# Optimization experiments

Hardware: AMD Instinct MI355X
Metric: run time of the kernel (lower is better)

Reference implementation:

```python
import jax, jax.numpy as jnp
import numpy as np

N_NODES = 100000
N_EDGES = 1600000
NFEAT, NHID, NCLASS = 128, 64, 40


def setup_inputs() -> dict:
    key = jax.random.key(0)
    k = jax.random.split(key, 6)
    x = jax.random.normal(k[0], (N_NODES, NFEAT), dtype=jnp.float32)
    edge_index = jax.random.randint(k[1], (2, N_EDGES), 0, N_NODES, dtype=jnp.int64)
    edge_weight = jax.random.uniform(k[2], (N_EDGES,), dtype=jnp.float32)
    # Glorot-style init as in PyG GCNConv.reset_parameters
    W1 = jax.random.normal(k[3], (NFEAT, NHID), dtype=jnp.float32) * (1.0 / np.sqrt(NFEAT))
    b1 = jnp.zeros((NHID,), dtype=jnp.float32)
    W2 = jax.random.normal(k[4], (NHID, NCLASS), dtype=jnp.float32) * (1.0 / np.sqrt(NHID))
    b2 = jnp.zeros((NCLASS,), dtype=jnp.float32)
    return {"x": x, "edge_index": edge_index, "edge_weight": edge_weight,
            "W1": W1, "b1": b1, "W2": W2, "b2": b2}


def _gcn_conv(x, edge_index, edge_weight, W, b):
    """PyG GCNConv: add self-loops, symmetric gcn_norm, linear, scatter-add, bias."""
    n = x.shape[0]
    loop = jnp.arange(n)
    row = jnp.concatenate([edge_index[0], loop])  # source nodes
    col = jnp.concatenate([edge_index[1], loop])  # target nodes
    w = jnp.concatenate([edge_weight, jnp.ones((n,), edge_weight.dtype)])
    deg = jax.ops.segment_sum(w, col, num_segments=n)          # [N]
    dinv = jnp.where(deg > 0, jax.lax.rsqrt(deg), 0.0)
    norm = dinv[row] * w * dinv[col]                           # [E+N]
    h = x @ W                                                  # [N, out]
    msg = norm[:, None] * h[row]                               # gather: [E+N, out]
    out = jax.ops.segment_sum(msg, col, num_segments=n)        # scatter-add: [N, out]
    return out + b


def reference(x, edge_index, edge_weight, W1, b1, W2, b2):
    h = jax.nn.relu(_gcn_conv(x, edge_index, edge_weight, W1, b1))
    # F.dropout with training=False is identity (eval mode)
    return _gcn_conv(h, edge_index, edge_weight, W2, b2)
```

## Files before the change

kernel.cpp:

```cpp
#include <hip/hip_runtime.h>
#include <hip/hip_bf16.h>

#define N_NODES 100000
#define N_EDGES 1600000
#define NFEAT 128
#define NHID 64
#define NCLASS 40
#define CAP 64

#define BIN_SHIFT 9
#define BIN_NODES 512
#define NBIN ((N_NODES + BIN_NODES - 1) / BIN_NODES)
#define SCAP 10240
#define CHUNK 4096
#define EPT 16
#define BIN_BLOCKS ((N_EDGES + CHUNK - 1) / CHUNK)
#define GEMM1_BLOCKS ((N_NODES + 63) / 64)

using frag_ab = __attribute__((ext_vector_type(8))) short;
using frag_cd = __attribute__((ext_vector_type(4))) float;


__device__ __forceinline__ unsigned pack2(float a, float b) {
    unsigned ua = __float_as_uint(a), ub = __float_as_uint(b);
    unsigned ra = (ua + 0x7FFFu + ((ua >> 16) & 1u)) >> 16;
    unsigned rb = (ub + 0x7FFFu + ((ub >> 16) & 1u)) >> 16;
    return ra | (rb << 16);
}
__device__ __forceinline__ unsigned short bf16rtn(float f) {
    unsigned u = __float_as_uint(f);
    return (unsigned short)((u + 0x7FFFu + ((u >> 16) & 1u)) >> 16);
}
__device__ __forceinline__ float lo16(unsigned w) { return __uint_as_float(w << 16); }
__device__ __forceinline__ float hi16(unsigned w) { return __uint_as_float(w & 0xFFFF0000u); }


__global__ __launch_bounds__(256) void fusedA_kernel(
        const int* __restrict__ ei, const float* __restrict__ ew,
        int* __restrict__ bincnt, uint2* __restrict__ staging,
        const float* __restrict__ x, const float* __restrict__ W1,
        unsigned short* __restrict__ h1b) {
    __shared__ unsigned short sm[16384];
    int t = threadIdx.x;

    if (blockIdx.x < BIN_BLOCKS) {
        int* lcnt  = (int*)sm;
        int* gbase = lcnt + NBIN;
        for (int i = t; i < NBIN; i += 256) lcnt[i] = 0;
        __syncthreads();

        int base = blockIdx.x * CHUNK;
        int c[EPT]; unsigned en[EPT];
#pragma unroll
        for (int u = 0; u < EPT; ++u) {
            int e = base + u * 256 + t;
            if (e < N_EDGES) {
                c[u] = ei[N_EDGES + e];
                unsigned wq = (unsigned)fminf(ew[e] * 32768.0f, 32767.0f);
                en[u] = ((unsigned)ei[e] << 15) | wq;
            } else {
                c[u] = -1;
            }
        }
#pragma unroll
        for (int u = 0; u < EPT; ++u)
            if (c[u] >= 0) atomicAdd(&lcnt[c[u] >> BIN_SHIFT], 1);
        __syncthreads();
        if (t < NBIN) {
            int n = lcnt[t];
            gbase[t] = (n > 0) ? atomicAdd(&bincnt[t], n) : 0;
        }
        __syncthreads();
        if (t < NBIN) lcnt[t] = 0;
        __syncthreads();
#pragma unroll
        for (int u = 0; u < EPT; ++u) {
            if (c[u] >= 0) {
                int b = c[u] >> BIN_SHIFT;
                int p = gbase[b] + atomicAdd(&lcnt[b], 1);
                if (p < SCAP)
                    staging[(size_t)b * SCAP + p] = make_uint2(en[u], (unsigned)c[u]);
            }
        }
        return;
    }

    int row0 = (blockIdx.x - BIN_BLOCKS) * 64;

#pragma unroll
    for (int p = 0; p < 4; ++p) {
        int id = p * 256 + t;
        int r = id >> 4;
        int c = id & 15;
        int gr = row0 + r; if (gr > N_NODES - 1) gr = N_NODES - 1;
        const float* src = x + (size_t)gr * NFEAT + c * 8;
        float4 f0 = *(const float4*)src;
        float4 f1 = *(const float4*)(src + 4);
        uint4 pk = make_uint4(pack2(f0.x, f0.y), pack2(f0.z, f0.w),
                              pack2(f1.x, f1.y), pack2(f1.z, f1.w));
        int cs = c ^ (r & 15);
        *(uint4*)(&sm[r * 128 + cs * 8]) = pk;
    }
#pragma unroll
    for (int p = 0; p < 4; ++p) {
        int id = p * 256 + t;
        int n = id >> 4;
        int c = id & 15;
        const float* wsrc = W1 + (size_t)(c * 8) * NHID + n;
        uint4 pk = make_uint4(pack2(wsrc[0 * NHID], wsrc[1 * NHID]),
                              pack2(wsrc[2 * NHID], wsrc[3 * NHID]),
                              pack2(wsrc[4 * NHID], wsrc[5 * NHID]),
                              pack2(wsrc[6 * NHID], wsrc[7 * NHID]));
        int cs = c ^ (n & 15);
        *(uint4*)(&sm[8192 + n * 128 + cs * 8]) = pk;
    }
    __syncthreads();

    int w = t >> 6, l = t & 63;
    int li = l & 15, q = l >> 4;
    int arow = w * 16 + li;

    frag_cd acc0 = {0.f, 0.f, 0.f, 0.f};
    frag_cd acc1 = {0.f, 0.f, 0.f, 0.f};
    frag_cd acc2 = {0.f, 0.f, 0.f, 0.f};
    frag_cd acc3 = {0.f, 0.f, 0.f, 0.f};

#pragma unroll
    for (int kc = 0; kc < 4; ++kc) {
        int cc = (kc * 4 + q) ^ li;
        frag_ab a  = *(const frag_ab*)(&sm[arow * 128 + cc * 8]);
        frag_ab b0 = *(const frag_ab*)(&sm[8192 + (0 * 16 + li) * 128 + cc * 8]);
        frag_ab b1 = *(const frag_ab*)(&sm[8192 + (1 * 16 + li) * 128 + cc * 8]);
        frag_ab b2 = *(const frag_ab*)(&sm[8192 + (2 * 16 + li) * 128 + cc * 8]);
        frag_ab b3 = *(const frag_ab*)(&sm[8192 + (3 * 16 + li) * 128 + cc * 8]);
        acc0 = __builtin_amdgcn_mfma_f32_16x16x32_bf16(a, b0, acc0, 0, 0, 0);
        acc1 = __builtin_amdgcn_mfma_f32_16x16x32_bf16(a, b1, acc1, 0, 0, 0);
        acc2 = __builtin_amdgcn_mfma_f32_16x16x32_bf16(a, b2, acc2, 0, 0, 0);
        acc3 = __builtin_amdgcn_mfma_f32_16x16x32_bf16(a, b3, acc3, 0, 0, 0);
    }

#pragma unroll
    for (int reg = 0; reg < 4; ++reg) {
        int rrow = row0 + w * 16 + q * 4 + reg;
        if (rrow < N_NODES) {
            unsigned short* dst = h1b + (size_t)rrow * NHID + li;
            dst[0]  = bf16rtn(acc0[reg]);
            dst[16] = bf16rtn(acc1[reg]);
            dst[32] = bf16rtn(acc2[reg]);
            dst[48] = bf16rtn(acc3[reg]);
        }
    }
}


__global__ __launch_bounds__(512) void place_kernel(const int* __restrict__ bincnt,
                                                    const uint2* __restrict__ staging,
                                                    unsigned* __restrict__ bucket,
                                                    int* __restrict__ cnt,
                                                    float* __restrict__ dinv,
                                                    int* __restrict__ ghist) {
    __shared__ int lpos[BIN_NODES];
    __shared__ float lws[BIN_NODES];
    __shared__ int lhist[CAP + 1];
    int b = blockIdx.x;
    int t = threadIdx.x;
    for (int i = t; i < BIN_NODES; i += 512) { lpos[i] = 0; lws[i] = 0.0f; }
    if (t <= CAP) lhist[t] = 0;
    __syncthreads();

    int nodebase = b << BIN_SHIFT;
    int n = bincnt[b];
    if (n > SCAP) n = SCAP;
    const uint2* st = staging + (size_t)b * SCAP;
    for (int i = t; i < n; i += 512) {
        uint2 en = st[i];
        int local = (int)en.y - nodebase;
        int p = atomicAdd(&lpos[local], 1);
        if (p < CAP) bucket[((size_t)en.y << 6) + p] = en.x;
        atomicAdd(&lws[local], (float)(en.x & 32767u) * (1.0f / 32768.0f));
    }
    __syncthreads();
    for (int i = t; i < BIN_NODES; i += 512) {
        int node = nodebase + i;
        if (node < N_NODES) {
            int d = min(lpos[i], CAP);
            cnt[node] = d;
            dinv[node] = rsqrtf(1.0f + lws[i]);
            atomicAdd(&lhist[d], 1);
        }
    }
    __syncthreads();
    if (t <= CAP) { int h = lhist[t]; if (h) atomicAdd(&ghist[t], h); }
}


__global__ __launch_bounds__(512) void perm_kernel(const int* __restrict__ cnt,
                                                   const int* __restrict__ ghist,
                                                   int* __restrict__ goffs,
                                                   int* __restrict__ perm) {
    __shared__ int base[CAP + 1];
    __shared__ int lh[CAP + 1];
    __shared__ int lbase[CAP + 1];
    int t = threadIdx.x;
    if (t <= CAP) lh[t] = 0;
    if (t == 0) {
        int s = 0;
        for (int d = 0; d <= CAP; ++d) { base[d] = s; s += ghist[d]; }
    }
    __syncthreads();
    int node = blockIdx.x * 512 + t;
    bool v = node < N_NODES;
    int d = 0, rank = 0;
    if (v) { d = cnt[node]; rank = atomicAdd(&lh[d], 1); }
    __syncthreads();
    if (t <= CAP) { int h = lh[t]; lbase[t] = h ? atomicAdd(&goffs[t], h) : 0; }
    __syncthreads();
    if (v) perm[base[d] + lbase[d] + rank] = node;
}


__global__ __launch_bounds__(256) void gather1_kernel(
        const int* __restrict__ cnt, const unsigned* __restrict__ bucket,
        const float* __restrict__ dinv, const unsigned short* __restrict__ h1b,
        const float* __restrict__ b1, unsigned short* __restrict__ relu1b,
        const int* __restrict__ perm) {
    int t = threadIdx.x;
    int lane = t & 63;
    int wave = t >> 6;
    int g = lane >> 3;
    int l = lane & 7;
    int slot = (blockIdx.x * 4 + wave) * 8 + g;
    bool nvalid = slot < N_NODES;
    int node = perm[nvalid ? slot : 0];
    int d = cnt[node];
    float dc = dinv[node];

    uint4 eb0 = *(const uint4*)(bucket + ((size_t)node << 6) + l * 8);
    uint4 eb1 = *(const uint4*)(bucket + ((size_t)node << 6) + l * 8 + 4);
    int rl[8]; float wl[8];
#pragma unroll
    for (int k = 0; k < 8; ++k) {
        unsigned e = (k < 4) ? ((const unsigned*)&eb0)[k] : ((const unsigned*)&eb1)[k - 4];
        int sl = l * 8 + k;
        bool ok = sl < d;
        int r = ok ? (int)(e >> 15) : 0;
        rl[k] = r;
        wl[k] = ok ? (float)(e & 32767u) * (1.0f / 32768.0f) * dinv[r] : 0.0f;
    }

    uint4 hs = *(const uint4*)(h1b + (size_t)node * NHID + l * 8);
    float acc[8];
#pragma unroll
    for (int k = 0; k < 4; ++k) {
        unsigned w = ((const unsigned*)&hs)[k];
        acc[2 * k] = dc * lo16(w);
        acc[2 * k + 1] = dc * hi16(w);
    }

    for (int j = 0; j < d; j += 8) {
        int src = (g << 3) + (j >> 3);
        int r[8]; float w[8];
#pragma unroll
        for (int k = 0; k < 8; ++k) { r[k] = __shfl(rl[k], src); w[k] = __shfl(wl[k], src); }
        uint4 v[8];
#pragma unroll
        for (int k = 0; k < 8; ++k)
            v[k] = *(const uint4*)(h1b + (size_t)r[k] * NHID + l * 8);
#pragma unroll
        for (int k = 0; k < 8; ++k) {
#pragma unroll
            for (int q = 0; q < 4; ++q) {
                unsigned ww = ((const unsigned*)&v[k])[q];
                acc[2 * q] += w[k] * lo16(ww);
                acc[2 * q + 1] += w[k] * hi16(ww);
            }
        }
    }
    if (nvalid) {
        float4 bv0 = *(const float4*)(b1 + l * 8);
        float4 bv1 = *(const float4*)(b1 + l * 8 + 4);
        float o0 = fmaxf(dc * acc[0] + bv0.x, 0.0f), o1 = fmaxf(dc * acc[1] + bv0.y, 0.0f);
        float o2 = fmaxf(dc * acc[2] + bv0.z, 0.0f), o3 = fmaxf(dc * acc[3] + bv0.w, 0.0f);
        float o4 = fmaxf(dc * acc[4] + bv1.x, 0.0f), o5 = fmaxf(dc * acc[5] + bv1.y, 0.0f);
        float o6 = fmaxf(dc * acc[6] + bv1.z, 0.0f), o7 = fmaxf(dc * acc[7] + bv1.w, 0.0f);
        uint4 pk = make_uint4(pack2(o0, o1), pack2(o2, o3), pack2(o4, o5), pack2(o6, o7));
        *(uint4*)(relu1b + (size_t)node * NHID + l * 8) = pk;
    }
}


__global__ __launch_bounds__(256) void gemm2_kernel(const unsigned short* __restrict__ relu1b,
                                                    const float* __restrict__ W2,
                                                    unsigned short* __restrict__ h2b) {
    __shared__ unsigned short sa[64 * 64];
    __shared__ unsigned short sb[48 * 64];
    int t = threadIdx.x;
    int row0 = blockIdx.x * 64;

#pragma unroll
    for (int p = 0; p < 2; ++p) {
        int id = p * 256 + t;
        int r = id >> 3, cj = id & 7;
        int gr = row0 + r; if (gr > N_NODES - 1) gr = N_NODES - 1;
        uint4 v = *(const uint4*)(relu1b + (size_t)gr * NHID + cj * 8);
        int cs = cj ^ (r & 7);
        *(uint4*)(&sa[r * 64 + cs * 8]) = v;
    }
    for (int id = t; id < 384; id += 256) {
        int n = id >> 3, cj = id & 7;
        uint4 v = make_uint4(0u, 0u, 0u, 0u);
        if (n < NCLASS) {
            const float* wsrc = W2 + (size_t)(cj * 8) * NCLASS + n;
            v = make_uint4(pack2(wsrc[0 * NCLASS], wsrc[1 * NCLASS]),
                           pack2(wsrc[2 * NCLASS], wsrc[3 * NCLASS]),
                           pack2(wsrc[4 * NCLASS], wsrc[5 * NCLASS]),
                           pack2(wsrc[6 * NCLASS], wsrc[7 * NCLASS]));
        }
        int cs = cj ^ (n & 7);
        *(uint4*)(&sb[n * 64 + cs * 8]) = v;
    }
    __syncthreads();

    int w = t >> 6, l = t & 63;
    int li = l & 15, q = l >> 4;
    int arow = w * 16 + li;

    frag_cd acc0 = {0.f, 0.f, 0.f, 0.f};
    frag_cd acc1 = {0.f, 0.f, 0.f, 0.f};
    frag_cd acc2 = {0.f, 0.f, 0.f, 0.f};

#pragma unroll
    for (int kc = 0; kc < 2; ++kc) {
        int cc = (kc * 4 + q) ^ (li & 7);
        frag_ab a  = *(const frag_ab*)(&sa[arow * 64 + cc * 8]);
        frag_ab b0 = *(const frag_ab*)(&sb[(0 + li) * 64 + cc * 8]);
        frag_ab b1 = *(const frag_ab*)(&sb[(16 + li) * 64 + cc * 8]);
        frag_ab b2 = *(const frag_ab*)(&sb[(32 + li) * 64 + cc * 8]);
        acc0 = __builtin_amdgcn_mfma_f32_16x16x32_bf16(a, b0, acc0, 0, 0, 0);
        acc1 = __builtin_amdgcn_mfma_f32_16x16x32_bf16(a, b1, acc1, 0, 0, 0);
        acc2 = __builtin_amdgcn_mfma_f32_16x16x32_bf16(a, b2, acc2, 0, 0, 0);
    }

#pragma unroll
    for (int reg = 0; reg < 4; ++reg) {
        int rrow = row0 + w * 16 + q * 4 + reg;
        if (rrow < N_NODES) {
            unsigned short* dst = h2b + (size_t)rrow * NCLASS;
            dst[li] = bf16rtn(acc0[reg]);
            dst[16 + li] = bf16rtn(acc1[reg]);
            if (li < 8) dst[32 + li] = bf16rtn(acc2[reg]);
        }
    }
}


__global__ __launch_bounds__(256) void gather2_kernel(
        const int* __restrict__ cnt, const unsigned* __restrict__ bucket,
        const float* __restrict__ dinv, const unsigned short* __restrict__ h2b,
        const float* __restrict__ b2, float* __restrict__ out,
        const int* __restrict__ perm) {
    int t = threadIdx.x;
    int lane = t & 63;
    int wave = t >> 6;
    int g = lane >> 4;
    int l = lane & 15;
    int slot = (blockIdx.x * 4 + wave) * 4 + g;
    bool nvalid = slot < N_NODES;
    int node = perm[nvalid ? slot : 0];
    int d = cnt[node];
    float dc = dinv[node];
    bool fvalid = (l < 10);

    uint4 eb = *(const uint4*)(bucket + ((size_t)node << 6) + l * 4);
    int rl[4]; float wl[4];
#pragma unroll
    for (int k = 0; k < 4; ++k) {
        unsigned e = ((const unsigned*)&eb)[k];
        int sl = l * 4 + k;
        bool ok = sl < d;
        int r = ok ? (int)(e >> 15) : 0;
        rl[k] = r;
        wl[k] = ok ? (float)(e & 32767u) * (1.0f / 32768.0f) * dinv[r] : 0.0f;
    }

    float acc[4] = {};
    int lc = fvalid ? l * 4 : 0;
    if (fvalid) {
        uint2 hs = *(const uint2*)(h2b + (size_t)node * NCLASS + lc);
        acc[0] = dc * lo16(hs.x); acc[1] = dc * hi16(hs.x);
        acc[2] = dc * lo16(hs.y); acc[3] = dc * hi16(hs.y);
    }

    for (int j = 0; j < d; j += 4) {
        int src = (g << 4) + (j >> 2);
        int r0 = __shfl(rl[0], src), r1 = __shfl(rl[1], src);
        int r2 = __shfl(rl[2], src), r3 = __shfl(rl[3], src);
        float w0 = __shfl(wl[0], src), w1 = __shfl(wl[1], src);
        float w2 = __shfl(wl[2], src), w3 = __shfl(wl[3], src);
        if (fvalid) {
            uint2 v0 = *(const uint2*)(h2b + (size_t)r0 * NCLASS + lc);
            uint2 v1 = *(const uint2*)(h2b + (size_t)r1 * NCLASS + lc);
            uint2 v2 = *(const uint2*)(h2b + (size_t)r2 * NCLASS + lc);
            uint2 v3 = *(const uint2*)(h2b + (size_t)r3 * NCLASS + lc);
            acc[0] += w0 * lo16(v0.x) + w1 * lo16(v1.x) + w2 * lo16(v2.x) + w3 * lo16(v3.x);
            acc[1] += w0 * hi16(v0.x) + w1 * hi16(v1.x) + w2 * hi16(v2.x) + w3 * hi16(v3.x);
            acc[2] += w0 * lo16(v0.y) + w1 * lo16(v1.y) + w2 * lo16(v2.y) + w3 * lo16(v3.y);
            acc[3] += w0 * hi16(v0.y) + w1 * hi16(v1.y) + w2 * hi16(v2.y) + w3 * hi16(v3.y);
        }
    }
    if (nvalid && fvalid) {
        float4 bv = *(const float4*)(b2 + l * 4);
        *(float4*)(out + (size_t)node * NCLASS + l * 4) =
            make_float4(dc * acc[0] + bv.x, dc * acc[1] + bv.y,
                        dc * acc[2] + bv.z, dc * acc[3] + bv.w);
    }
}


extern "C" void kernel_launch(void* const* d_in, const int* in_sizes, int n_in,
                              void* d_out, int out_size, void* d_ws, size_t ws_size,
                              hipStream_t stream) {
    const float* x  = (const float*)d_in[0];
    const int*   ei = (const int*)d_in[1];
    const float* ew = (const float*)d_in[2];
    const float* W1 = (const float*)d_in[3];
    const float* b1 = (const float*)d_in[4];
    const float* W2 = (const float*)d_in[5];
    const float* b2 = (const float*)d_in[6];
    float* out = (float*)d_out;

    int*            bincnt  = (int*)d_ws;
    int*            ghist   = bincnt + 256;
    int*            goffs   = ghist + 65;
    int*            cnt     = bincnt + 512;
    float*          dinv    = (float*)(cnt + 100352);
    unsigned*       bucket  = (unsigned*)(dinv + 100352);
    unsigned short* h1b     = (unsigned short*)(bucket + (size_t)N_NODES * CAP);
    unsigned short* region2 = h1b + (size_t)N_NODES * NHID;
    uint2*          staging = (uint2*)region2;
    unsigned short* relu1b  = region2;
    int*            perm    = (int*)(relu1b + (size_t)N_NODES * NHID);
    unsigned short* h2b     = h1b;

    hipMemsetAsync(bincnt, 0, 512 * sizeof(int), stream);

    fusedA_kernel<<<BIN_BLOCKS + GEMM1_BLOCKS, 256, 0, stream>>>(
        ei, ew, bincnt, staging, x, W1, h1b);
    place_kernel<<<NBIN, 512, 0, stream>>>(bincnt, staging, bucket, cnt, dinv, ghist);
    perm_kernel<<<NBIN, 512, 0, stream>>>(cnt, ghist, goffs, perm);

    gather1_kernel<<<(N_NODES + 31) / 32, 256, 0, stream>>>(
        cnt, bucket, dinv, h1b, b1, relu1b, perm);

    gemm2_kernel<<<(N_NODES + 63) / 64, 256, 0, stream>>>(relu1b, W2, h2b);
    gather2_kernel<<<(N_NODES + 15) / 16, 256, 0, stream>>>(
        cnt, bucket, dinv, h2b, b2, out, perm);
}
```

Measured before the change: 255.7 us.

## Fuse layer-1 gather with layer-2 GEMM and split binning from GEMM1

The layer-1 aggregation now writes its ReLU output as a bf16 tile into shared memory, and the same block immediately runs the W2 MFMA product. The result is scattered to h2b through perm, so the relu1b round trip through global memory and a kernel launch both go away. The fused binning+GEMM1 kernel is split back into separate bin and gemm1 kernels. This removes the branch divergence between block types but loses any overlap the fused launch gave, and each g1g2 block reloads W2 into shared memory.

```diff
diff --git a/kernel.cpp b/kernel.cpp
--- a/kernel.cpp
+++ b/kernel.cpp
@@ -14,8 +14,6 @@
 #define SCAP 10240
 #define CHUNK 4096
 #define EPT 16
-#define BIN_BLOCKS ((N_EDGES + CHUNK - 1) / CHUNK)
-#define GEMM1_BLOCKS ((N_NODES + 63) / 64)
 
 using frag_ab = __attribute__((ext_vector_type(8))) short;
 using frag_cd = __attribute__((ext_vector_type(4))) float;
@@ -35,57 +33,124 @@
 __device__ __forceinline__ float hi16(unsigned w) { return __uint_as_float(w & 0xFFFF0000u); }
 
 
-__global__ __launch_bounds__(256) void fusedA_kernel(
-        const int* __restrict__ ei, const float* __restrict__ ew,
-        int* __restrict__ bincnt, uint2* __restrict__ staging,
-        const float* __restrict__ x, const float* __restrict__ W1,
-        unsigned short* __restrict__ h1b) {
+__global__ __launch_bounds__(256) void bin_kernel(const int* __restrict__ ei,
+                                                  const float* __restrict__ ew,
+                                                  int* __restrict__ bincnt,
+                                                  uint2* __restrict__ staging) {
+    __shared__ int lcnt[NBIN];
+    __shared__ int gbase[NBIN];
+    int t = threadIdx.x;
+    for (int i = t; i < NBIN; i += 256) lcnt[i] = 0;
+    __syncthreads();
+
+    int base = blockIdx.x * CHUNK;
+    int c[EPT]; unsigned en[EPT];
+#pragma unroll
+    for (int u = 0; u < EPT; ++u) {
+        int e = base + u * 256 + t;
+        if (e < N_EDGES) {
+            c[u] = ei[N_EDGES + e];
+            unsigned wq = (unsigned)fminf(ew[e] * 32768.0f, 32767.0f);
+            en[u] = ((unsigned)ei[e] << 15) | wq;
+        } else {
+            c[u] = -1;
+        }
+    }
+#pragma unroll
+    for (int u = 0; u < EPT; ++u)
+        if (c[u] >= 0) atomicAdd(&lcnt[c[u] >> BIN_SHIFT], 1);
+    __syncthreads();
+    if (t < NBIN) {
+        int n = lcnt[t];
+        gbase[t] = (n > 0) ? atomicAdd(&bincnt[t], n) : 0;
+    }
+    __syncthreads();
+    if (t < NBIN) lcnt[t] = 0;
+    __syncthreads();
+#pragma unroll
+    for (int u = 0; u < EPT; ++u) {
+        if (c[u] >= 0) {
+            int b = c[u] >> BIN_SHIFT;
+            int p = gbase[b] + atomicAdd(&lcnt[b], 1);
+            if (p < SCAP)
+                staging[(size_t)b * SCAP + p] = make_uint2(en[u], (unsigned)c[u]);
+        }
+    }
+}
+
+
+__global__ __launch_bounds__(512) void place_kernel(const int* __restrict__ bincnt,
+                                                    const uint2* __restrict__ staging,
+                                                    unsigned* __restrict__ bucket,
+                                                    int* __restrict__ cnt,
+                                                    float* __restrict__ dinv,
+                                                    int* __restrict__ ghist) {
+    __shared__ int lpos[BIN_NODES];
+    __shared__ float lws[BIN_NODES];
+    __shared__ int lhist[CAP + 1];
+    int b = blockIdx.x;
+    int t = threadIdx.x;
+    for (int i = t; i < BIN_NODES; i += 512) { lpos[i] = 0; lws[i] = 0.0f; }
+    if (t <= CAP) lhist[t] = 0;
+    __syncthreads();
+
+    int nodebase = b << BIN_SHIFT;
+    int n = bincnt[b];
+    if (n > SCAP) n = SCAP;
+    const uint2* st = staging + (size_t)b * SCAP;
+    for (int i = t; i < n; i += 512) {
+        uint2 en = st[i];
+        int local = (int)en.y - nodebase;
+        int p = atomicAdd(&lpos[local], 1);
+        if (p < CAP) bucket[((size_t)en.y << 6) + p] = en.x;
+        atomicAdd(&lws[local], (float)(en.x & 32767u) * (1.0f / 32768.0f));
+    }
+    __syncthreads();
+    for (int i = t; i < BIN_NODES; i += 512) {
+        int node = nodebase + i;
+        if (node < N_NODES) {
+            int d = min(lpos[i], CAP);
+            cnt[node] = d;
+            dinv[node] = rsqrtf(1.0f + lws[i]);
+            atomicAdd(&lhist[d], 1);
+        }
+    }
+    __syncthreads();
+    if (t <= CAP) { int h = lhist[t]; if (h) atomicAdd(&ghist[t], h); }
+}
+
+
+__global__ __launch_bounds__(512) void perm_kernel(const int* __restrict__ cnt,
+                                                   const int* __restrict__ ghist,
+                                                   int* __restrict__ goffs,
+                                                   int* __restrict__ perm) {
+    __shared__ int base[CAP + 1];
+    __shared__ int lh[CAP + 1];
+    __shared__ int lbase[CAP + 1];
+    int t = threadIdx.x;
+    if (t <= CAP) lh[t] = 0;
+    if (t == 0) {
+        int s = 0;
+        for (int d = 0; d <= CAP; ++d) { base[d] = s; s += ghist[d]; }
+    }
+    __syncthreads();
+    int node = blockIdx.x * 512 + t;
+    bool v = node < N_NODES;
+    int d = 0, rank = 0;
+    if (v) { d = cnt[node]; rank = atomicAdd(&lh[d], 1); }
+    __syncthreads();
+    if (t <= CAP) { int h = lh[t]; lbase[t] = h ? atomicAdd(&goffs[t], h) : 0; }
+    __syncthreads();
+    if (v) perm[base[d] + lbase[d] + rank] = node;
+}
+
+
+__global__ __launch_bounds__(256) void gemm1_kernel(const float* __restrict__ x,
+                                                    const float* __restrict__ W1,
+                                                    unsigned short* __restrict__ h1b) {
     __shared__ unsigned short sm[16384];
     int t = threadIdx.x;
-
-    if (blockIdx.x < BIN_BLOCKS) {
-        int* lcnt  = (int*)sm;
-        int* gbase = lcnt + NBIN;
-        for (int i = t; i < NBIN; i += 256) lcnt[i] = 0;
-        __syncthreads();
-
-        int base = blockIdx.x * CHUNK;
-        int c[EPT]; unsigned en[EPT];
-#pragma unroll
-        for (int u = 0; u < EPT; ++u) {
-            int e = base + u * 256 + t;
-            if (e < N_EDGES) {
-                c[u] = ei[N_EDGES + e];
-                unsigned wq = (unsigned)fminf(ew[e] * 32768.0f, 32767.0f);
-                en[u] = ((unsigned)ei[e] << 15) | wq;
-            } else {
-                c[u] = -1;
-            }
-        }
-#pragma unroll
-        for (int u = 0; u < EPT; ++u)
-            if (c[u] >= 0) atomicAdd(&lcnt[c[u] >> BIN_SHIFT], 1);
-        __syncthreads();
-        if (t < NBIN) {
-            int n = lcnt[t];
-            gbase[t] = (n > 0) ? atomicAdd(&bincnt[t], n) : 0;
-        }
-        __syncthreads();
-        if (t < NBIN) lcnt[t] = 0;
-        __syncthreads();
-#pragma unroll
-        for (int u = 0; u < EPT; ++u) {
-            if (c[u] >= 0) {
-                int b = c[u] >> BIN_SHIFT;
-                int p = gbase[b] + atomicAdd(&lcnt[b], 1);
-                if (p < SCAP)
-                    staging[(size_t)b * SCAP + p] = make_uint2(en[u], (unsigned)c[u]);
-            }
-        }
-        return;
-    }
-
-    int row0 = (blockIdx.x - BIN_BLOCKS) * 64;
+    int row0 = blockIdx.x * 64;
 
 #pragma unroll
     for (int p = 0; p < 4; ++p) {
@@ -153,160 +218,25 @@
 }
 
 
-__global__ __launch_bounds__(512) void place_kernel(const int* __restrict__ bincnt,
-                                                    const uint2* __restrict__ staging,
-                                                    unsigned* __restrict__ bucket,
-                                                    int* __restrict__ cnt,
-                                                    float* __restrict__ dinv,
-                                                    int* __restrict__ ghist) {
-    __shared__ int lpos[BIN_NODES];
-    __shared__ float lws[BIN_NODES];
-    __shared__ int lhist[CAP + 1];
-    int b = blockIdx.x;
-    int t = threadIdx.x;
-    for (int i = t; i < BIN_NODES; i += 512) { lpos[i] = 0; lws[i] = 0.0f; }
-    if (t <= CAP) lhist[t] = 0;
-    __syncthreads();
-
-    int nodebase = b << BIN_SHIFT;
-    int n = bincnt[b];
-    if (n > SCAP) n = SCAP;
-    const uint2* st = staging + (size_t)b * SCAP;
-    for (int i = t; i < n; i += 512) {
-        uint2 en = st[i];
-        int local = (int)en.y - nodebase;
-        int p = atomicAdd(&lpos[local], 1);
-        if (p < CAP) bucket[((size_t)en.y << 6) + p] = en.x;
-        atomicAdd(&lws[local], (float)(en.x & 32767u) * (1.0f / 32768.0f));
-    }
-    __syncthreads();
-    for (int i = t; i < BIN_NODES; i += 512) {
-        int node = nodebase + i;
-        if (node < N_NODES) {
-            int d = min(lpos[i], CAP);
-            cnt[node] = d;
-            dinv[node] = rsqrtf(1.0f + lws[i]);
-            atomicAdd(&lhist[d], 1);
-        }
-    }
-    __syncthreads();
-    if (t <= CAP) { int h = lhist[t]; if (h) atomicAdd(&ghist[t], h); }
-}
-
-
-__global__ __launch_bounds__(512) void perm_kernel(const int* __restrict__ cnt,
-                                                   const int* __restrict__ ghist,
-                                                   int* __restrict__ goffs,
-                                                   int* __restrict__ perm) {
-    __shared__ int base[CAP + 1];
-    __shared__ int lh[CAP + 1];
-    __shared__ int lbase[CAP + 1];
-    int t = threadIdx.x;
-    if (t <= CAP) lh[t] = 0;
-    if (t == 0) {
-        int s = 0;
-        for (int d = 0; d <= CAP; ++d) { base[d] = s; s += ghist[d]; }
-    }
-    __syncthreads();
-    int node = blockIdx.x * 512 + t;
-    bool v = node < N_NODES;
-    int d = 0, rank = 0;
-    if (v) { d = cnt[node]; rank = atomicAdd(&lh[d], 1); }
-    __syncthreads();
-    if (t <= CAP) { int h = lh[t]; lbase[t] = h ? atomicAdd(&goffs[t], h) : 0; }
-    __syncthreads();
-    if (v) perm[base[d] + lbase[d] + rank] = node;
-}
-
-
-__global__ __launch_bounds__(256) void gather1_kernel(
+__global__ __launch_bounds__(256) void g1g2_kernel(
         const int* __restrict__ cnt, const unsigned* __restrict__ bucket,
         const float* __restrict__ dinv, const unsigned short* __restrict__ h1b,
-        const float* __restrict__ b1, unsigned short* __restrict__ relu1b,
-        const int* __restrict__ perm) {
+        const float* __restrict__ b1, const float* __restrict__ W2,
+        unsigned short* __restrict__ h2b, const int* __restrict__ perm) {
+    __shared__ unsigned short sa[32 * 64];
+    __shared__ unsigned short sb[64 * 64];
     int t = threadIdx.x;
     int lane = t & 63;
     int wave = t >> 6;
     int g = lane >> 3;
     int l = lane & 7;
-    int slot = (blockIdx.x * 4 + wave) * 8 + g;
+    int slot = blockIdx.x * 32 + wave * 8 + g;
     bool nvalid = slot < N_NODES;
     int node = perm[nvalid ? slot : 0];
     int d = cnt[node];
     float dc = dinv[node];
 
-    uint4 eb0 = *(const uint4*)(bucket + ((size_t)node << 6) + l * 8);
-    uint4 eb1 = *(const uint4*)(bucket + ((size_t)node << 6) + l * 8 + 4);
-    int rl[8]; float wl[8];
-#pragma unroll
-    for (int k = 0; k < 8; ++k) {
-        unsigned e = (k < 4) ? ((const unsigned*)&eb0)[k] : ((const unsigned*)&eb1)[k - 4];
-        int sl = l * 8 + k;
-        bool ok = sl < d;
-        int r = ok ? (int)(e >> 15) : 0;
-        rl[k] = r;
-        wl[k] = ok ? (float)(e & 32767u) * (1.0f / 32768.0f) * dinv[r] : 0.0f;
-    }
-
-    uint4 hs = *(const uint4*)(h1b + (size_t)node * NHID + l * 8);
-    float acc[8];
-#pragma unroll
-    for (int k = 0; k < 4; ++k) {
-        unsigned w = ((const unsigned*)&hs)[k];
-        acc[2 * k] = dc * lo16(w);
-        acc[2 * k + 1] = dc * hi16(w);
-    }
-
-    for (int j = 0; j < d; j += 8) {
-        int src = (g << 3) + (j >> 3);
-        int r[8]; float w[8];
-#pragma unroll
-        for (int k = 0; k < 8; ++k) { r[k] = __shfl(rl[k], src); w[k] = __shfl(wl[k], src); }
-        uint4 v[8];
-#pragma unroll
-        for (int k = 0; k < 8; ++k)
-            v[k] = *(const uint4*)(h1b + (size_t)r[k] * NHID + l * 8);
-#pragma unroll
-        for (int k = 0; k < 8; ++k) {
-#pragma unroll
-            for (int q = 0; q < 4; ++q) {
-                unsigned ww = ((const unsigned*)&v[k])[q];
-                acc[2 * q] += w[k] * lo16(ww);
-                acc[2 * q + 1] += w[k] * hi16(ww);
-            }
-        }
-    }
-    if (nvalid) {
-        float4 bv0 = *(const float4*)(b1 + l * 8);
-        float4 bv1 = *(const float4*)(b1 + l * 8 + 4);
-        float o0 = fmaxf(dc * acc[0] + bv0.x, 0.0f), o1 = fmaxf(dc * acc[1] + bv0.y, 0.0f);
-        float o2 = fmaxf(dc * acc[2] + bv0.z, 0.0f), o3 = fmaxf(dc * acc[3] + bv0.w, 0.0f);
-        float o4 = fmaxf(dc * acc[4] + bv1.x, 0.0f), o5 = fmaxf(dc * acc[5] + bv1.y, 0.0f);
-        float o6 = fmaxf(dc * acc[6] + bv1.z, 0.0f), o7 = fmaxf(dc * acc[7] + bv1.w, 0.0f);
-        uint4 pk = make_uint4(pack2(o0, o1), pack2(o2, o3), pack2(o4, o5), pack2(o6, o7));
-        *(uint4*)(relu1b + (size_t)node * NHID + l * 8) = pk;
-    }
-}
-
-
-__global__ __launch_bounds__(256) void gemm2_kernel(const unsigned short* __restrict__ relu1b,
-                                                    const float* __restrict__ W2,
-                                                    unsigned short* __restrict__ h2b) {
-    __shared__ unsigned short sa[64 * 64];
-    __shared__ unsigned short sb[48 * 64];
-    int t = threadIdx.x;
-    int row0 = blockIdx.x * 64;
-
-#pragma unroll
-    for (int p = 0; p < 2; ++p) {
-        int id = p * 256 + t;
-        int r = id >> 3, cj = id & 7;
-        int gr = row0 + r; if (gr > N_NODES - 1) gr = N_NODES - 1;
-        uint4 v = *(const uint4*)(relu1b + (size_t)gr * NHID + cj * 8);
-        int cs = cj ^ (r & 7);
-        *(uint4*)(&sa[r * 64 + cs * 8]) = v;
-    }
-    for (int id = t; id < 384; id += 256) {
+    for (int id = t; id < 512; id += 256) {
         int n = id >> 3, cj = id & 7;
         uint4 v = make_uint4(0u, 0u, 0u, 0u);
         if (n < NCLASS) {
@@ -319,36 +249,90 @@
         int cs = cj ^ (n & 7);
         *(uint4*)(&sb[n * 64 + cs * 8]) = v;
     }
-    __syncthreads();
-
-    int w = t >> 6, l = t & 63;
-    int li = l & 15, q = l >> 4;
-    int arow = w * 16 + li;
-
-    frag_cd acc0 = {0.f, 0.f, 0.f, 0.f};
-    frag_cd acc1 = {0.f, 0.f, 0.f, 0.f};
-    frag_cd acc2 = {0.f, 0.f, 0.f, 0.f};
-
+
+    uint4 eb0 = *(const uint4*)(bucket + ((size_t)node << 6) + l * 8);
+    uint4 eb1 = *(const uint4*)(bucket + ((size_t)node << 6) + l * 8 + 4);
+    int rl[8]; float wl[8];
+#pragma unroll
+    for (int k = 0; k < 8; ++k) {
+        unsigned e = (k < 4) ? ((const unsigned*)&eb0)[k] : ((const unsigned*)&eb1)[k - 4];
+        int sl = l * 8 + k;
+        bool ok = sl < d;
+        int r = ok ? (int)(e >> 15) : 0;
+        rl[k] = r;
+        wl[k] = ok ? (float)(e & 32767u) * (1.0f / 32768.0f) * dinv[r] : 0.0f;
+    }
+
+    uint4 hs = *(const uint4*)(h1b + (size_t)node * NHID + l * 8);
+    float acc[8];
+#pragma unroll
+    for (int k = 0; k < 4; ++k) {
+        unsigned w = ((const unsigned*)&hs)[k];
+        acc[2 * k] = dc * lo16(w);
+        acc[2 * k + 1] = dc * hi16(w);
+    }
+
+    for (int j = 0; j < d; j += 8) {
+        int src = (g << 3) + (j >> 3);
+        int r[8]; float w[8];
+#pragma unroll
+        for (int k = 0; k < 8; ++k) { r[k] = __shfl(rl[k], src); w[k] = __shfl(wl[k], src); }
+        uint4 v[8];
+#pragma unroll
+        for (int k = 0; k < 8; ++k)
+            v[k] = *(const uint4*)(h1b + (size_t)r[k] * NHID + l * 8);
+#pragma unroll
+        for (int k = 0; k < 8; ++k) {
+#pragma unroll
+            for (int q = 0; q < 4; ++q) {
+                unsigned ww = ((const unsigned*)&v[k])[q];
+                acc[2 * q] += w[k] * lo16(ww);
+                acc[2 * q + 1] += w[k] * hi16(ww);
+            }
+        }
+    }
+
+    {
+        float4 bv0 = *(const float4*)(b1 + l * 8);
+        float4 bv1 = *(const float4*)(b1 + l * 8 + 4);
+        float o0 = fmaxf(dc * acc[0] + bv0.x, 0.0f), o1 = fmaxf(dc * acc[1] + bv0.y, 0.0f);
+        float o2 = fmaxf(dc * acc[2] + bv0.z, 0.0f), o3 = fmaxf(dc * acc[3] + bv0.w, 0.0f);
+        float o4 = fmaxf(dc * acc[4] + bv1.x, 0.0f), o5 = fmaxf(dc * acc[5] + bv1.y, 0.0f);
+        float o6 = fmaxf(dc * acc[6] + bv1.z, 0.0f), o7 = fmaxf(dc * acc[7] + bv1.w, 0.0f);
+        uint4 pk = make_uint4(pack2(o0, o1), pack2(o2, o3), pack2(o4, o5), pack2(o6, o7));
+        int r = wave * 8 + g;
+        int cs = l ^ (r & 7);
+        *(uint4*)(&sa[r * 64 + cs * 8]) = pk;
+    }
+    __syncthreads();
+
+    int li = lane & 15, q = lane >> 4;
+    int arow = (wave & 1) * 16 + li;
+    int ct0 = (wave >> 1) * 2;
+
+    frag_cd c0 = {0.f, 0.f, 0.f, 0.f};
+    frag_cd c1 = {0.f, 0.f, 0.f, 0.f};
 #pragma unroll
     for (int kc = 0; kc < 2; ++kc) {
         int cc = (kc * 4 + q) ^ (li & 7);
         frag_ab a  = *(const frag_ab*)(&sa[arow * 64 + cc * 8]);
-        frag_ab b0 = *(const frag_ab*)(&sb[(0 + li) * 64 + cc * 8]);
-        frag_ab b1 = *(const frag_ab*)(&sb[(16 + li) * 64 + cc * 8]);
-        frag_ab b2 = *(const frag_ab*)(&sb[(32 + li) * 64 + cc * 8]);
-        acc0 = __builtin_amdgcn_mfma_f32_16x16x32_bf16(a, b0, acc0, 0, 0, 0);
-        acc1 = __builtin_amdgcn_mfma_f32_16x16x32_bf16(a, b1, acc1, 0, 0, 0);
-        acc2 = __builtin_amdgcn_mfma_f32_16x16x32_bf16(a, b2, acc2, 0, 0, 0);
+        frag_ab b0 = *(const frag_ab*)(&sb[(ct0 * 16 + li) * 64 + cc * 8]);
+        frag_ab b1f = *(const frag_ab*)(&sb[((ct0 + 1) * 16 + li) * 64 + cc * 8]);
+        c0 = __builtin_amdgcn_mfma_f32_16x16x32_bf16(a, b0, c0, 0, 0, 0);
+        c1 = __builtin_amdgcn_mfma_f32_16x16x32_bf16(a, b1f, c1, 0, 0, 0);
     }
 
 #pragma unroll
     for (int reg = 0; reg < 4; ++reg) {
-        int rrow = row0 + w * 16 + q * 4 + reg;
-        if (rrow < N_NODES) {
-            unsigned short* dst = h2b + (size_t)rrow * NCLASS;
-            dst[li] = bf16rtn(acc0[reg]);
-            dst[16 + li] = bf16rtn(acc1[reg]);
-            if (li < 8) dst[32 + li] = bf16rtn(acc2[reg]);
+        int rr = (wave & 1) * 16 + q * 4 + reg;
+        int oslot = blockIdx.x * 32 + rr;
+        if (oslot < N_NODES) {
+            int onode = perm[oslot];
+            unsigned short* dst = h2b + (size_t)onode * NCLASS;
+            int col0 = ct0 * 16 + li;
+            int col1 = (ct0 + 1) * 16 + li;
+            if (col0 < NCLASS) dst[col0] = bf16rtn(c0[reg]);
+            if (col1 < NCLASS) dst[col1] = bf16rtn(c1[reg]);
         }
     }
 }
@@ -438,21 +422,20 @@
     unsigned short* h1b     = (unsigned short*)(bucket + (size_t)N_NODES * CAP);
     unsigned short* region2 = h1b + (size_t)N_NODES * NHID;
     uint2*          staging = (uint2*)region2;
-    unsigned short* relu1b  = region2;
-    int*            perm    = (int*)(relu1b + (size_t)N_NODES * NHID);
-    unsigned short* h2b     = h1b;
+    unsigned short* h2b     = region2;
+    int*            perm    = (int*)(region2 + (size_t)N_NODES * NCLASS);
 
     hipMemsetAsync(bincnt, 0, 512 * sizeof(int), stream);
 
-    fusedA_kernel<<<BIN_BLOCKS + GEMM1_BLOCKS, 256, 0, stream>>>(
-        ei, ew, bincnt, staging, x, W1, h1b);
+    bin_kernel<<<(N_EDGES + CHUNK - 1) / CHUNK, 256, 0, stream>>>(ei, ew, bincnt, staging);
     place_kernel<<<NBIN, 512, 0, stream>>>(bincnt, staging, bucket, cnt, dinv, ghist);
     perm_kernel<<<NBIN, 512, 0, stream>>>(cnt, ghist, goffs, perm);
 
-    gather1_kernel<<<(N_NODES + 31) / 32, 256, 0, stream>>>(
-        cnt, bucket, dinv, h1b, b1, relu1b, perm);
-
-    gemm2_kernel<<<(N_NODES + 63) / 64, 256, 0, stream>>>(relu1b, W2, h2b);
+    gemm1_kernel<<<(N_NODES + 63) / 64, 256, 0, stream>>>(x, W1, h1b);
+
+    g1g2_kernel<<<(N_NODES + 31) / 32, 256, 0, stream>>>(
+        cnt, bucket, dinv, h1b, b1, W2, h2b, perm);
+
     gather2_kernel<<<(N_NODES + 15) / 16, 256, 0, stream>>>(
         cnt, bucket, dinv, h2b, b2, out, perm);
 }
```

Result: slower. 268.6 us (+5.0%).

## Fold degree-sorted permutation into place kernel, split binning from GEMM1

Applied to the files above, without the earlier changes.

Merges perm_kernel into place_kernel by computing a per-bin local degree sort instead of a global one, which removes one launch and the global histogram and offset atomics. The fused bin+GEMM1 kernel is split into separate bin_kernel and gemm1_kernel launches. The gather kernels also skip loading bucket slots beyond the node's degree. The trade-off is that the degree ordering now holds only within 512-node bins, so wave load balance in the gathers may be weaker, and the binning and GEMM1 work no longer overlap in one grid.

```diff
diff --git a/kernel.cpp b/kernel.cpp
--- a/kernel.cpp
+++ b/kernel.cpp
@@ -14,8 +14,6 @@
 #define SCAP 10240
 #define CHUNK 4096
 #define EPT 16
-#define BIN_BLOCKS ((N_EDGES + CHUNK - 1) / CHUNK)
-#define GEMM1_BLOCKS ((N_NODES + 63) / 64)
 
 using frag_ab = __attribute__((ext_vector_type(8))) short;
 using frag_cd = __attribute__((ext_vector_type(4))) float;
@@ -35,57 +33,110 @@
 __device__ __forceinline__ float hi16(unsigned w) { return __uint_as_float(w & 0xFFFF0000u); }
 
 
-__global__ __launch_bounds__(256) void fusedA_kernel(
-        const int* __restrict__ ei, const float* __restrict__ ew,
-        int* __restrict__ bincnt, uint2* __restrict__ staging,
-        const float* __restrict__ x, const float* __restrict__ W1,
-        unsigned short* __restrict__ h1b) {
+__global__ __launch_bounds__(256) void bin_kernel(const int* __restrict__ ei,
+                                                  const float* __restrict__ ew,
+                                                  int* __restrict__ bincnt,
+                                                  uint2* __restrict__ staging) {
+    __shared__ int lcnt[NBIN];
+    __shared__ int gbase[NBIN];
+    int t = threadIdx.x;
+    for (int i = t; i < NBIN; i += 256) lcnt[i] = 0;
+    __syncthreads();
+
+    int base = blockIdx.x * CHUNK;
+    int c[EPT]; unsigned en[EPT];
+#pragma unroll
+    for (int u = 0; u < EPT; ++u) {
+        int e = base + u * 256 + t;
+        if (e < N_EDGES) {
+            c[u] = ei[N_EDGES + e];
+            unsigned wq = (unsigned)fminf(ew[e] * 32768.0f, 32767.0f);
+            en[u] = ((unsigned)ei[e] << 15) | wq;
+        } else {
+            c[u] = -1;
+        }
+    }
+#pragma unroll
+    for (int u = 0; u < EPT; ++u)
+        if (c[u] >= 0) atomicAdd(&lcnt[c[u] >> BIN_SHIFT], 1);
+    __syncthreads();
+    if (t < NBIN) {
+        int n = lcnt[t];
+        gbase[t] = (n > 0) ? atomicAdd(&bincnt[t], n) : 0;
+    }
+    __syncthreads();
+    if (t < NBIN) lcnt[t] = 0;
+    __syncthreads();
+#pragma unroll
+    for (int u = 0; u < EPT; ++u) {
+        if (c[u] >= 0) {
+            int b = c[u] >> BIN_SHIFT;
+            int p = gbase[b] + atomicAdd(&lcnt[b], 1);
+            if (p < SCAP)
+                staging[(size_t)b * SCAP + p] = make_uint2(en[u], (unsigned)c[u]);
+        }
+    }
+}
+
+
+__global__ __launch_bounds__(512) void place_kernel(const int* __restrict__ bincnt,
+                                                    const uint2* __restrict__ staging,
+                                                    unsigned* __restrict__ bucket,
+                                                    int* __restrict__ cnt,
+                                                    float* __restrict__ dinv,
+                                                    int* __restrict__ perm) {
+    __shared__ int lpos[BIN_NODES];
+    __shared__ float lws[BIN_NODES];
+    __shared__ int lhist[CAP + 1];
+    __shared__ int lbase[CAP + 1];
+    int b = blockIdx.x;
+    int t = threadIdx.x;
+    for (int i = t; i < BIN_NODES; i += 512) { lpos[i] = 0; lws[i] = 0.0f; }
+    if (t <= CAP) lhist[t] = 0;
+    __syncthreads();
+
+    int nodebase = b << BIN_SHIFT;
+    int n = bincnt[b];
+    if (n > SCAP) n = SCAP;
+    const uint2* st = staging + (size_t)b * SCAP;
+    for (int i = t; i < n; i += 512) {
+        uint2 en = st[i];
+        int local = (int)en.y - nodebase;
+        int p = atomicAdd(&lpos[local], 1);
+        if (p < CAP) bucket[((size_t)en.y << 6) + p] = en.x;
+        atomicAdd(&lws[local], (float)(en.x & 32767u) * (1.0f / 32768.0f));
+    }
+    __syncthreads();
+
+    int node = nodebase + t;
+    bool v = node < N_NODES;
+    int d = 0;
+    if (v) {
+        d = min(lpos[t], CAP);
+        cnt[node] = d;
+        dinv[node] = rsqrtf(1.0f + lws[t]);
+        atomicAdd(&lhist[d], 1);
+    }
+    __syncthreads();
+    if (t == 0) {
+        int s = 0;
+        for (int dd = 0; dd <= CAP; ++dd) { lbase[dd] = s; s += lhist[dd]; }
+    }
+    if (t <= CAP) lhist[t] = 0;
+    __syncthreads();
+    if (v) {
+        int rank = atomicAdd(&lhist[d], 1);
+        perm[nodebase + lbase[d] + rank] = node;
+    }
+}
+
+
+__global__ __launch_bounds__(256) void gemm1_kernel(const float* __restrict__ x,
+                                                    const float* __restrict__ W1,
+                                                    unsigned short* __restrict__ h1b) {
     __shared__ unsigned short sm[16384];
     int t = threadIdx.x;
-
-    if (blockIdx.x < BIN_BLOCKS) {
-        int* lcnt  = (int*)sm;
-        int* gbase = lcnt + NBIN;
-        for (int i = t; i < NBIN; i += 256) lcnt[i] = 0;
-        __syncthreads();
-
-        int base = blockIdx.x * CHUNK;
-        int c[EPT]; unsigned en[EPT];
-#pragma unroll
-        for (int u = 0; u < EPT; ++u) {
-            int e = base + u * 256 + t;
-            if (e < N_EDGES) {
-                c[u] = ei[N_EDGES + e];
-                unsigned wq = (unsigned)fminf(ew[e] * 32768.0f, 32767.0f);
-                en[u] = ((unsigned)ei[e] << 15) | wq;
-            } else {
-                c[u] = -1;
-            }
-        }
-#pragma unroll
-        for (int u = 0; u < EPT; ++u)
-            if (c[u] >= 0) atomicAdd(&lcnt[c[u] >> BIN_SHIFT], 1);
-        __syncthreads();
-        if (t < NBIN) {
-            int n = lcnt[t];
-            gbase[t] = (n > 0) ? atomicAdd(&bincnt[t], n) : 0;
-        }
-        __syncthreads();
-        if (t < NBIN) lcnt[t] = 0;
-        __syncthreads();
-#pragma unroll
-        for (int u = 0; u < EPT; ++u) {
-            if (c[u] >= 0) {
-                int b = c[u] >> BIN_SHIFT;
-                int p = gbase[b] + atomicAdd(&lcnt[b], 1);
-                if (p < SCAP)
-                    staging[(size_t)b * SCAP + p] = make_uint2(en[u], (unsigned)c[u]);
-            }
-        }
-        return;
-    }
-
-    int row0 = (blockIdx.x - BIN_BLOCKS) * 64;
+    int row0 = blockIdx.x * 64;
 
 #pragma unroll
     for (int p = 0; p < 4; ++p) {
@@ -153,72 +204,6 @@
 }
 
 
-__global__ __launch_bounds__(512) void place_kernel(const int* __restrict__ bincnt,
-                                                    const uint2* __restrict__ staging,
-                                                    unsigned* __restrict__ bucket,
-                                                    int* __restrict__ cnt,
-                                                    float* __restrict__ dinv,
-                                                    int* __restrict__ ghist) {
-    __shared__ int lpos[BIN_NODES];
-    __shared__ float lws[BIN_NODES];
-    __shared__ int lhist[CAP + 1];
-    int b = blockIdx.x;
-    int t = threadIdx.x;
-    for (int i = t; i < BIN_NODES; i += 512) { lpos[i] = 0; lws[i] = 0.0f; }
-    if (t <= CAP) lhist[t] = 0;
-    __syncthreads();
-
-    int nodebase = b << BIN_SHIFT;
-    int n = bincnt[b];
-    if (n > SCAP) n = SCAP;
-    const uint2* st = staging + (size_t)b * SCAP;
-    for (int i = t; i < n; i += 512) {
-        uint2 en = st[i];
-        int local = (int)en.y - nodebase;
-        int p = atomicAdd(&lpos[local], 1);
-        if (p < CAP) bucket[((size_t)en.y << 6) + p] = en.x;
-        atomicAdd(&lws[local], (float)(en.x & 32767u) * (1.0f / 32768.0f));
-    }
-    __syncthreads();
-    for (int i = t; i < BIN_NODES; i += 512) {
-        int node = nodebase + i;
-        if (node < N_NODES) {
-            int d = min(lpos[i], CAP);
-            cnt[node] = d;
-            dinv[node] = rsqrtf(1.0f + lws[i]);
-            atomicAdd(&lhist[d], 1);
-        }
-    }
-    __syncthreads();
-    if (t <= CAP) { int h = lhist[t]; if (h) atomicAdd(&ghist[t], h); }
-}
-
-
-__global__ __launch_bounds__(512) void perm_kernel(const int* __restrict__ cnt,
-                                                   const int* __restrict__ ghist,
-                                                   int* __restrict__ goffs,
-                                                   int* __restrict__ perm) {
-    __shared__ int base[CAP + 1];
-    __shared__ int lh[CAP + 1];
-    __shared__ int lbase[CAP + 1];
-    int t = threadIdx.x;
-    if (t <= CAP) lh[t] = 0;
-    if (t == 0) {
-        int s = 0;
-        for (int d = 0; d <= CAP; ++d) { base[d] = s; s += ghist[d]; }
-    }
-    __syncthreads();
-    int node = blockIdx.x * 512 + t;
-    bool v = node < N_NODES;
-    int d = 0, rank = 0;
-    if (v) { d = cnt[node]; rank = atomicAdd(&lh[d], 1); }
-    __syncthreads();
-    if (t <= CAP) { int h = lh[t]; lbase[t] = h ? atomicAdd(&goffs[t], h) : 0; }
-    __syncthreads();
-    if (v) perm[base[d] + lbase[d] + rank] = node;
-}
-
-
 __global__ __launch_bounds__(256) void gather1_kernel(
         const int* __restrict__ cnt, const unsigned* __restrict__ bucket,
         const float* __restrict__ dinv, const unsigned short* __restrict__ h1b,
@@ -235,8 +220,9 @@
     int d = cnt[node];
     float dc = dinv[node];
 
-    uint4 eb0 = *(const uint4*)(bucket + ((size_t)node << 6) + l * 8);
-    uint4 eb1 = *(const uint4*)(bucket + ((size_t)node << 6) + l * 8 + 4);
+    uint4 eb0 = make_uint4(0u, 0u, 0u, 0u), eb1 = make_uint4(0u, 0u, 0u, 0u);
+    if (l * 8 < d)     eb0 = *(const uint4*)(bucket + ((size_t)node << 6) + l * 8);
+    if (l * 8 + 4 < d) eb1 = *(const uint4*)(bucket + ((size_t)node << 6) + l * 8 + 4);
     int rl[8]; float wl[8];
 #pragma unroll
     for (int k = 0; k < 8; ++k) {
@@ -371,7 +357,8 @@
     float dc = dinv[node];
     bool fvalid = (l < 10);
 
-    uint4 eb = *(const uint4*)(bucket + ((size_t)node << 6) + l * 4);
+    uint4 eb = make_uint4(0u, 0u, 0u, 0u);
+    if (l * 4 < d) eb = *(const uint4*)(bucket + ((size_t)node << 6) + l * 4);
     int rl[4]; float wl[4];
 #pragma unroll
     for (int k = 0; k < 4; ++k) {
@@ -430,25 +417,22 @@
     float* out = (float*)d_out;
 
     int*            bincnt  = (int*)d_ws;
-    int*            ghist   = bincnt + 256;
-    int*            goffs   = ghist + 65;
-    int*            cnt     = bincnt + 512;
+    int*            cnt     = bincnt + 256;
     float*          dinv    = (float*)(cnt + 100352);
-    unsigned*       bucket  = (unsigned*)(dinv + 100352);
+    int*            perm    = (int*)(dinv + 100352);
+    unsigned*       bucket  = (unsigned*)(perm + 100352);
     unsigned short* h1b     = (unsigned short*)(bucket + (size_t)N_NODES * CAP);
     unsigned short* region2 = h1b + (size_t)N_NODES * NHID;
     uint2*          staging = (uint2*)region2;
     unsigned short* relu1b  = region2;
-    int*            perm    = (int*)(relu1b + (size_t)N_NODES * NHID);
     unsigned short* h2b     = h1b;
 
-    hipMemsetAsync(bincnt, 0, 512 * sizeof(int), stream);
-
-    fusedA_kernel<<<BIN_BLOCKS + GEMM1_BLOCKS, 256, 0, stream>>>(
-        ei, ew, bincnt, staging, x, W1, h1b);
-    place_kernel<<<NBIN, 512, 0, stream>>>(bincnt, staging, bucket, cnt, dinv, ghist);
-    perm_kernel<<<NBIN, 512, 0, stream>>>(cnt, ghist, goffs, perm);
-
+    hipMemsetAsync(bincnt, 0, 256 * sizeof(int), stream);
+
+    bin_kernel<<<(N_EDGES + CHUNK - 1) / CHUNK, 256, 0, stream>>>(ei, ew, bincnt, staging);
+    place_kernel<<<NBIN, 512, 0, stream>>>(bincnt, staging, bucket, cnt, dinv, perm);
+
+    gemm1_kernel<<<(N_NODES + 63) / 64, 256, 0, stream>>>(x, W1, h1b);
     gather1_kernel<<<(N_NODES + 31) / 32, 256, 0, stream>>>(
         cnt, bucket, dinv, h1b, b1, relu1b, perm);
 
```

Result: slower. 265.9 us (+4.0%).
